# Kernel tuning notes

Measured on AMD Instinct MI355X. Metric: run time of the kernel, lower is better.

Reference implementation:

```python
import jax, jax.numpy as jnp
import numpy as np

VOX = 64      # vox_size
KS = 21       # smooth_ks (odd -> 'SAME' == pad ks//2)
SIGMA = 3.0   # smooth_sigma


def smoothing_kernel():
    # normalized 1D gaussian used separably along the 3 voxel axes
    x = jnp.arange(KS, dtype=jnp.float32) - (KS - 1) / 2.0
    g = jnp.exp(-(x * x) / (2.0 * SIGMA * SIGMA))
    return g / g.sum()


def pc_voxels(pc, size):
    """Trilinear scatter of points in [-0.5,0.5]^3 into a [B,size,size,size] grid."""
    B, N, _ = pc.shape
    g = (pc + 0.5) * (size - 1)            # grid coords
    fl = jnp.floor(g)
    idx = fl.astype(jnp.int32)             # [B,N,3] lower corner
    frac = g - fl                          # trilinear fractions
    # 8 corner offsets in {0,1}^3
    offs = jnp.array([[(i >> 2) & 1, (i >> 1) & 1, i & 1] for i in range(8)], dtype=jnp.int32)
    pos = idx[:, :, None, :] + offs[None, None]                       # [B,N,8,3]
    w = jnp.prod(jnp.where(offs[None, None].astype(bool),
                           frac[:, :, None, :], 1.0 - frac[:, :, None, :]), axis=-1)  # [B,N,8]
    inb = jnp.all((pos >= 0) & (pos < size), axis=-1)
    w = jnp.where(inb, w, 0.0)
    posc = jnp.clip(pos, 0, size - 1)
    # voxel layout vox[b, z, y, x]; pc columns are (x, y, z)
    flat = posc[..., 2] * (size * size) + posc[..., 1] * size + posc[..., 0]
    vox = jnp.zeros((B, size * size * size), pc.dtype)
    vox = vox.at[jnp.arange(B)[:, None, None], flat].add(w)
    return jnp.clip(vox.reshape(B, size, size, size), 0.0, 1.0)


def voxels_smooth(v, g1d, scale):
    """Separable 3D Gaussian smoothing + per-batch scale, clamped to [0,1]."""
    x = v[:, None]  # NCDHW, C=1
    ks = g1d.shape[0]
    for kshape in ((1, 1, ks, 1, 1), (1, 1, 1, ks, 1), (1, 1, 1, 1, ks)):
        x = jax.lax.conv_general_dilated(
            x, g1d.reshape(kshape), (1, 1, 1), 'SAME',
            dimension_numbers=('NCDHW', 'OIDHW', 'NCDHW'))
    x = x[:, 0] * scale[:, None, None, None]
    return jnp.clip(x, 0.0, 1.0)


def drc_prob(v):
    """DRC ray-termination probabilities along depth (axis 1)."""
    trans = jnp.cumprod(1.0 - v, axis=1)                                   # [B,D,H,W]
    tshift = jnp.concatenate([jnp.ones_like(trans[:, :1]), trans[:, :-1]], axis=1)
    stop = v * tshift                                                      # stop at voxel d
    esc = trans[:, -1:]                                                    # ray escapes
    return jnp.concatenate([stop, esc], axis=1)                            # [B,D+1,H,W]


def reference(pc, rotation, scale):
    pc_t = jnp.einsum('bni,bji->bnj', pc, rotation)   # camera transform: pc @ R^T
    vox = pc_voxels(pc_t, VOX)
    sm = voxels_smooth(vox, smoothing_kernel(), scale)
    prob = drc_prob(sm)
    proj = prob[:, :-1].sum(1)[:, ::-1, :]            # sum over depth, flip rows
    return proj


def setup_inputs() -> dict:
    key = jax.random.key(0)
    k1, k2, k3 = jax.random.split(key, 3)
    B, N = 32, 65536
    pc = jax.random.uniform(k1, (B, N, 3), jnp.float32) - 0.5   # points in [-0.5, 0.5]
    q, _ = jnp.linalg.qr(jax.random.normal(k2, (B, 3, 3), jnp.float32))  # random rotations
    scale = 0.5 + jax.random.uniform(k3, (B,), jnp.float32)
    return {"pc": pc, "rotation": q, "scale": scale}
```

## Files before the change

kernel.cpp:

```cpp
#include <hip/hip_runtime.h>

#define NB    32
#define NP    65536
#define SZ    64
#define SZ3   (SZ * SZ * SZ)
#define KS    21
#define HALF  10
#define NBIN2 130
#define CAP2  1280
#define FXS   960.0f

typedef _Float16 half8_t __attribute__((ext_vector_type(8)));
typedef _Float16 half4_t __attribute__((ext_vector_type(4)));
typedef float    f32x4_t __attribute__((ext_vector_type(4)));

__device__ __forceinline__ int swz(int row, int col) {
    return (row << 6) + ((((col >> 3) ^ (row & 7))) << 3) + (col & 7);
}

__device__ __forceinline__ void weights_reg(float* w) {
    float sum = 0.0f;
#pragma unroll
    for (int k = 0; k < KS; ++k) {
        float d = (float)k - (float)HALF;
        w[k] = expf(-d * d / 18.0f);
        sum += w[k];
    }
#pragma unroll
    for (int k = 0; k < KS; ++k) w[k] /= sum;
}

__device__ __forceinline__ void fma4(float4& a, float t, const float4& v) {
    a.x = fmaf(t, v.x, a.x); a.y = fmaf(t, v.y, a.y);
    a.z = fmaf(t, v.z, a.z); a.w = fmaf(t, v.w, a.w);
}

__device__ __forceinline__ unsigned pack_fx(float g) {
    float c = fminf(fmaxf(g, -2.0f), 65.0f);
    return (unsigned)__float2uint_rn((c + 2.0f) * FXS);
}

__global__ void fill_kernel(const float* __restrict__ pc,
                            const float* __restrict__ rot,
                            int* __restrict__ cur,
                            uint2* __restrict__ binned,
                            _Float16* __restrict__ Gg) {
    __shared__ int h[4][NBIN2];
    __shared__ int woff[4][NBIN2];
    __shared__ int lbase[NBIN2];
    int base = blockIdx.x * 1024;
    int b = base >> 16;
    int wv = threadIdx.x >> 6;
    for (int i = threadIdx.x; i < 4 * NBIN2; i += 256) h[i / NBIN2][i % NBIN2] = 0;
    __syncthreads();
    const float* R = rot + b * 9;
    const float4* p4 = (const float4*)(pc + (size_t)base * 3);
    float4 f0 = p4[threadIdx.x * 3 + 0];
    float4 f1 = p4[threadIdx.x * 3 + 1];
    float4 f2 = p4[threadIdx.x * 3 + 2];
    float px[4] = {f0.x, f0.w, f1.z, f2.y};
    float py[4] = {f0.y, f1.x, f1.w, f2.z};
    float pz[4] = {f0.z, f1.y, f2.x, f2.w};
    uint2 pk[4];
    int bin0[4], bin1[4], lp0[4], lp1[4];
#pragma unroll
    for (int j = 0; j < 4; ++j) {
        float g0 = (R[0] * px[j] + R[1] * py[j] + R[2] * pz[j] + 0.5f) * 63.0f;
        float g1 = (R[3] * px[j] + R[4] * py[j] + R[5] * pz[j] + 0.5f) * 63.0f;
        float g2 = (R[6] * px[j] + R[7] * py[j] + R[8] * pz[j] + 0.5f) * 63.0f;
        int i2 = (int)floorf(g2);
        int i1 = (int)floorf(g1);
        bool zv = (i2 >= -1 && i2 <= 63);
        int h0 = ((unsigned)i1       < 64u) ? (i1 >> 5)       : -1;
        int h1 = ((unsigned)(i1 + 1) < 64u) ? ((i1 + 1) >> 5) : -1;
        if (h1 == h0) h1 = -1;
        bin0[j] = (zv && h0 >= 0) ? ((i2 + 1) * 2 + h0) : -1;
        bin1[j] = (zv && h1 >= 0) ? ((i2 + 1) * 2 + h1) : -1;
        pk[j] = make_uint2(pack_fx(g0) | (pack_fx(g1) << 16), pack_fx(g2));
        if (bin0[j] >= 0) lp0[j] = atomicAdd(&h[wv][bin0[j]], 1);
        if (bin1[j] >= 0) lp1[j] = atomicAdd(&h[wv][bin1[j]], 1);
    }
    __syncthreads();
    if (threadIdx.x < NBIN2) {
        int t = threadIdx.x;
        int s0 = h[0][t], s1 = h[1][t], s2 = h[2][t], s3 = h[3][t];
        int tot = s0 + s1 + s2 + s3;
        lbase[t] = tot ? atomicAdd(&cur[b * NBIN2 + t], tot) : 0;
        woff[0][t] = 0; woff[1][t] = s0; woff[2][t] = s0 + s1; woff[3][t] = s0 + s1 + s2;
    }
    __syncthreads();
#pragma unroll
    for (int j = 0; j < 4; ++j) {
        if (bin0[j] >= 0) {
            int pos = lbase[bin0[j]] + woff[wv][bin0[j]] + lp0[j];
            if (pos < CAP2)
                binned[(size_t)(b * NBIN2 + bin0[j]) * CAP2 + pos] = pk[j];
        }
        if (bin1[j] >= 0) {
            int pos = lbase[bin1[j]] + woff[wv][bin1[j]] + lp1[j];
            if (pos < CAP2)
                binned[(size_t)(b * NBIN2 + bin1[j]) * CAP2 + pos] = pk[j];
        }
    }
    if (blockIdx.x == 0) {
        float w[KS];
        weights_reg(w);
        for (int i = threadIdx.x; i < 4096; i += 256) {
            int d = (i >> 6) - (i & 63) + HALF;
            Gg[i] = ((unsigned)d < (unsigned)KS) ? (_Float16)w[d] : (_Float16)0.0f;
        }
    }
}

__global__ void __launch_bounds__(128) splat_blur(const uint2* __restrict__ binned,
                                                  const int* __restrict__ cur,
                                                  const _Float16* __restrict__ Gg,
                                                  _Float16* __restrict__ vox) {
    __shared__ __align__(16) char smem[25088];
    int tid = threadIdx.x;
    int w = tid >> 6, lane = tid & 63;
    int idx = blockIdx.x;
    int b = idx >> 6;
    int k = (idx + (b << 3)) & 63;
    int z = (k & 1) ? (31 - (k >> 1)) : (32 + (k >> 1));
    int q = lane >> 4, c = lane & 15;

    _Float16* Ay = (_Float16*)(smem + w * 4224);
    _Float16* Bx = (_Float16*)(smem + 8448 + w * 8320);
    _Float16* P  = (_Float16*)smem;
    _Float16* T  = (_Float16*)(smem + 8448);

    {
        int4 z4 = {0, 0, 0, 0};
        int4* a4 = (int4*)Ay;
        for (int i = lane; i < 4224 / 16; i += 64) a4[i] = z4;
        int4* b4 = (int4*)Bx;
        for (int i = lane; i < 8320 / 16; i += 64) b4[i] = z4;
    }

    half8_t gf[4][2];
#pragma unroll
    for (int ni = 0; ni < 4; ++ni)
#pragma unroll
        for (int hh = 0; hh < 2; ++hh)
            gf[ni][hh] = *(const half8_t*)&Gg[(ni * 16 + c) * 64 + hh * 32 + q * 8];

    int c0 = min(cur[b * NBIN2 + 2 * z + w],       CAP2);
    int c1 = min(cur[b * NBIN2 + 2 * (z + 1) + w], CAP2);
    const uint2* s0 = binned + (size_t)(b * NBIN2 + 2 * z + w) * CAP2;
    const uint2* s1 = binned + (size_t)(b * NBIN2 + 2 * (z + 1) + w) * CAP2;
    int n = c0 + c1;

    f32x4_t acc[2][4];
#pragma unroll
    for (int ml = 0; ml < 2; ++ml)
#pragma unroll
        for (int ni = 0; ni < 4; ++ni) acc[ml][ni] = (f32x4_t){0.f, 0.f, 0.f, 0.f};

    int iters = (n + 63) >> 6;
    uint2 nxtA = make_uint2(0u, 0u), nxtB = make_uint2(0u, 0u);
    {
        int i0g = lane;
        if (i0g < n) nxtA = (i0g < c0) ? s0[i0g] : s1[i0g - c0];
        int i1g = 64 + lane;
        if (i1g < n) nxtB = (i1g < c0) ? s0[i1g] : s1[i1g - c0];
    }
    for (int it = 0; it < iters; ++it) {
        uint2 pk = nxtA;
        nxtA = nxtB;
        nxtB = make_uint2(0u, 0u);
        int ni2 = (it + 2) * 64 + lane;
        if (ni2 < n) nxtB = (ni2 < c0) ? s0[ni2] : s1[ni2 - c0];

        float gx = (float)(pk.x & 0xffffu) * (1.0f / FXS) - 2.0f;
        float gy = (float)(pk.x >> 16)     * (1.0f / FXS) - 2.0f;
        float gz = (float)(pk.y & 0xffffu) * (1.0f / FXS) - 2.0f;
        float f0 = floorf(gx), f1 = floorf(gy);
        int   i0 = (int)f0,    i1 = (int)f1;
        float r0 = gx - f0,    r1f = gy - f1;
        float az = fmaxf(0.0f, 1.0f - fabsf(gz - (float)z));
        int rlo = i1 - (w << 5), rhi = i1 + 1 - (w << 5);
        int alo = ((unsigned)rlo < 32u) ? rlo : 32;
        int ahi = ((unsigned)rhi < 32u) ? rhi : 32;
        int xlo = ((unsigned)i0       < 64u) ? i0       : 64;
        int xhi = ((unsigned)(i0 + 1) < 64u) ? (i0 + 1) : 64;
        Ay[swz(alo, lane)] = (_Float16)(az * (1.0f - r1f));
        Ay[swz(ahi, lane)] = (_Float16)(az * r1f);
        Bx[swz(xlo, lane)] = (_Float16)(1.0f - r0);
        Bx[swz(xhi, lane)] = (_Float16)r0;
#pragma unroll
        for (int hh = 0; hh < 2; ++hh) {
            half8_t af[2], bf[4];
#pragma unroll
            for (int ml = 0; ml < 2; ++ml)
                af[ml] = *(const half8_t*)&Ay[swz(ml * 16 + c, hh * 32 + q * 8)];
#pragma unroll
            for (int ni = 0; ni < 4; ++ni)
                bf[ni] = *(const half8_t*)&Bx[swz(ni * 16 + c, hh * 32 + q * 8)];
#pragma unroll
            for (int ml = 0; ml < 2; ++ml)
#pragma unroll
                for (int ni = 0; ni < 4; ++ni)
                    acc[ml][ni] = __builtin_amdgcn_mfma_f32_16x16x32_f16(
                        af[ml], bf[ni], acc[ml][ni], 0, 0, 0);
        }
        Ay[swz(alo, lane)] = (_Float16)0.0f;
        Ay[swz(ahi, lane)] = (_Float16)0.0f;
        Bx[swz(xlo, lane)] = (_Float16)0.0f;
        Bx[swz(xhi, lane)] = (_Float16)0.0f;
    }

    __syncthreads();

#pragma unroll
    for (int ml = 0; ml < 2; ++ml)
#pragma unroll
        for (int ni = 0; ni < 4; ++ni)
#pragma unroll
            for (int r = 0; r < 4; ++r)
                P[swz((w << 5) + ml * 16 + q * 4 + r, ni * 16 + c)] =
                    (_Float16)fminf(fmaxf(acc[ml][ni][r], 0.0f), 1.0f);
    __syncthreads();

    f32x4_t a2[2][4];
#pragma unroll
    for (int ml = 0; ml < 2; ++ml)
#pragma unroll
        for (int ni = 0; ni < 4; ++ni) a2[ml][ni] = (f32x4_t){0.f, 0.f, 0.f, 0.f};
#pragma unroll
    for (int hh = 0; hh < 2; ++hh) {
        half8_t af[2];
#pragma unroll
        for (int ml = 0; ml < 2; ++ml)
            af[ml] = *(const half8_t*)&P[swz(((w << 1) + ml) * 16 + c, hh * 32 + q * 8)];
#pragma unroll
        for (int ml = 0; ml < 2; ++ml)
#pragma unroll
            for (int ni = 0; ni < 4; ++ni)
                a2[ml][ni] = __builtin_amdgcn_mfma_f32_16x16x32_f16(
                    af[ml], gf[ni][hh], a2[ml][ni], 0, 0, 0);
    }
#pragma unroll
    for (int ml = 0; ml < 2; ++ml)
#pragma unroll
        for (int ni = 0; ni < 4; ++ni) {
            half4_t pkd;
#pragma unroll
            for (int r = 0; r < 4; ++r) pkd[r] = (_Float16)a2[ml][ni][r];
            *(half4_t*)&T[swz(ni * 16 + c, ((w << 1) + ml) * 16 + q * 4)] = pkd;
        }
    __syncthreads();

    f32x4_t a3[2][4];
#pragma unroll
    for (int ml = 0; ml < 2; ++ml)
#pragma unroll
        for (int ni = 0; ni < 4; ++ni) a3[ml][ni] = (f32x4_t){0.f, 0.f, 0.f, 0.f};
#pragma unroll
    for (int hh = 0; hh < 2; ++hh) {
        half8_t bf[4];
#pragma unroll
        for (int ni = 0; ni < 4; ++ni)
            bf[ni] = *(const half8_t*)&T[swz(ni * 16 + c, hh * 32 + q * 8)];
#pragma unroll
        for (int ml = 0; ml < 2; ++ml)
#pragma unroll
            for (int ni = 0; ni < 4; ++ni)
                a3[ml][ni] = __builtin_amdgcn_mfma_f32_16x16x32_f16(
                    gf[(w << 1) + ml][hh], bf[ni], a3[ml][ni], 0, 0, 0);
    }

    _Float16* dst = vox + ((size_t)b << 18) + ((size_t)z << 12);
#pragma unroll
    for (int ml = 0; ml < 2; ++ml)
#pragma unroll
        for (int ni = 0; ni < 4; ++ni)
#pragma unroll
            for (int r = 0; r < 4; ++r)
                dst[(((w << 5) + ml * 16 + q * 4 + r) << 6) + ni * 16 + c] =
                    (_Float16)a3[ml][ni][r];
}

__global__ void convz_drc_kernel(const _Float16* __restrict__ in,
                                 const float* __restrict__ scale,
                                 float* __restrict__ out) {
    __shared__ float sraw[640 + SZ * SZ + 640];
    __shared__ float c[SZ * SZ];
    __shared__ float segS[4][64], segT[4][64];
    float* s = sraw + 640;
    int b = blockIdx.x >> 6, y = blockIdx.x & 63;

    for (int i = threadIdx.x; i < 640; i += 256) {
        sraw[i] = 0.0f;
        sraw[640 + SZ * SZ + i] = 0.0f;
    }
    const _Float16* base = in + ((size_t)b << 18) + (y << 6);
#pragma unroll
    for (int g = 0; g < 4; ++g) {
        int cell = g * 256 + threadIdx.x;
        int z = cell >> 4, xc = (cell & 15) << 2;
        half4_t v = *(const half4_t*)&base[((size_t)z << 12) + xc];
        float4 f = make_float4((float)v[0], (float)v[1], (float)v[2], (float)v[3]);
        *(float4*)&s[(z << 6) + xc] = f;
    }
    __syncthreads();

    float w[KS];
    weights_reg(w);

    {
        int z0 = (threadIdx.x >> 4) << 2;
        int xc = (threadIdx.x & 15) << 2;
        float4 a0 = {0,0,0,0}, a1 = {0,0,0,0}, a2 = {0,0,0,0}, a3 = {0,0,0,0};
#pragma unroll
        for (int d = 0; d < 24; ++d) {
            int zz = z0 - HALF + d;
            float4 v = *(const float4*)&s[(zz << 6) + xc];
            if (d <= 20)           fma4(a0, w[d],     v);
            if (d >= 1 && d <= 21) fma4(a1, w[d - 1], v);
            if (d >= 2 && d <= 22) fma4(a2, w[d - 2], v);
            if (d >= 3)            fma4(a3, w[d - 3], v);
        }
        *(float4*)&c[((z0 + 0) << 6) + xc] = a0;
        *(float4*)&c[((z0 + 1) << 6) + xc] = a1;
        *(float4*)&c[((z0 + 2) << 6) + xc] = a2;
        *(float4*)&c[((z0 + 3) << 6) + xc] = a3;
    }
    __syncthreads();

    {
        int x = threadIdx.x & 63, seg = threadIdx.x >> 6;
        float sc = scale[b];
        float trans = 1.0f, sum = 0.0f;
#pragma unroll
        for (int zz = 0; zz < 16; ++zz) {
            int z = seg * 16 + zz;
            float v = fminf(fmaxf(c[(z << 6) + x] * sc, 0.0f), 1.0f);
            sum += v * trans;
            trans *= 1.0f - v;
        }
        segS[seg][x] = sum;
        segT[seg][x] = trans;
    }
    __syncthreads();
    if (threadIdx.x < 64) {
        int x = threadIdx.x;
        float t = 1.0f, S = 0.0f;
#pragma unroll
        for (int sgi = 0; sgi < 4; ++sgi) { S += segS[sgi][x] * t; t *= segT[sgi][x]; }
        out[(b << 12) + ((63 - y) << 6) + x] = S;
    }
}

extern "C" void kernel_launch(void* const* d_in, const int* in_sizes, int n_in,
                              void* d_out, int out_size, void* d_ws, size_t ws_size,
                              hipStream_t stream) {
    const float* pc    = (const float*)d_in[0];
    const float* rot   = (const float*)d_in[1];
    const float* scale = (const float*)d_in[2];
    float* out = (float*)d_out;

    _Float16* vox    = (_Float16*)d_ws;
    uint2*    binned = (uint2*)((char*)d_ws + (size_t)NB * SZ3 * sizeof(_Float16));
    _Float16* Gg     = (_Float16*)((char*)binned + (size_t)NB * NBIN2 * CAP2 * sizeof(uint2));
    int*      cur    = (int*)((char*)Gg + 64 * 64 * sizeof(_Float16));

    hipMemsetAsync(cur, 0, NB * NBIN2 * sizeof(int), stream);

    fill_kernel     <<<NB * NP / 1024, 256, 0, stream>>>(pc, rot, cur, binned, Gg);
    splat_blur      <<<NB * SZ, 128, 0, stream>>>(binned, cur, Gg, vox);
    convz_drc_kernel<<<NB * SZ, 256, 0, stream>>>(vox, scale, out);
}
```

Baseline: 123.8 us.

## Bin points into 32x32 quadrants and use four waves per splat block

```diff
diff --git a/kernel.cpp b/kernel.cpp
--- a/kernel.cpp
+++ b/kernel.cpp
@@ -6,8 +6,8 @@
 #define SZ3   (SZ * SZ * SZ)
 #define KS    21
 #define HALF  10
-#define NBIN2 130
-#define CAP2  1280
+#define NBINQ 260
+#define CAPQ  1024
 #define FXS   960.0f
 
 typedef _Float16 half8_t __attribute__((ext_vector_type(8)));
@@ -45,13 +45,13 @@
                             int* __restrict__ cur,
                             uint2* __restrict__ binned,
                             _Float16* __restrict__ Gg) {
-    __shared__ int h[4][NBIN2];
-    __shared__ int woff[4][NBIN2];
-    __shared__ int lbase[NBIN2];
+    __shared__ int hist[4][NBINQ];
+    __shared__ int woff[4][NBINQ];
+    __shared__ int lbase[NBINQ];
     int base = blockIdx.x * 1024;
     int b = base >> 16;
     int wv = threadIdx.x >> 6;
-    for (int i = threadIdx.x; i < 4 * NBIN2; i += 256) h[i / NBIN2][i % NBIN2] = 0;
+    for (int i = threadIdx.x; i < 4 * NBINQ; i += 256) ((int*)hist)[i] = 0;
     __syncthreads();
     const float* R = rot + b * 9;
     const float4* p4 = (const float4*)(pc + (size_t)base * 3);
@@ -62,46 +62,48 @@
     float py[4] = {f0.y, f1.x, f1.w, f2.z};
     float pz[4] = {f0.z, f1.y, f2.x, f2.w};
     uint2 pk[4];
-    int bin0[4], bin1[4], lp0[4], lp1[4];
+    int bn[16], lp[16];
 #pragma unroll
     for (int j = 0; j < 4; ++j) {
         float g0 = (R[0] * px[j] + R[1] * py[j] + R[2] * pz[j] + 0.5f) * 63.0f;
         float g1 = (R[3] * px[j] + R[4] * py[j] + R[5] * pz[j] + 0.5f) * 63.0f;
         float g2 = (R[6] * px[j] + R[7] * py[j] + R[8] * pz[j] + 0.5f) * 63.0f;
-        int i2 = (int)floorf(g2);
-        int i1 = (int)floorf(g1);
+        int i2 = (int)floorf(g2), i1 = (int)floorf(g1), i0 = (int)floorf(g0);
         bool zv = (i2 >= -1 && i2 <= 63);
-        int h0 = ((unsigned)i1       < 64u) ? (i1 >> 5)       : -1;
-        int h1 = ((unsigned)(i1 + 1) < 64u) ? ((i1 + 1) >> 5) : -1;
-        if (h1 == h0) h1 = -1;
-        bin0[j] = (zv && h0 >= 0) ? ((i2 + 1) * 2 + h0) : -1;
-        bin1[j] = (zv && h1 >= 0) ? ((i2 + 1) * 2 + h1) : -1;
+        int ys[2], xs[2];
+        ys[0] = ((unsigned)i1       < 64u) ? (i1 >> 5)       : -1;
+        ys[1] = ((unsigned)(i1 + 1) < 64u) ? ((i1 + 1) >> 5) : -1;
+        if (ys[1] == ys[0]) ys[1] = -1;
+        xs[0] = ((unsigned)i0       < 64u) ? (i0 >> 5)       : -1;
+        xs[1] = ((unsigned)(i0 + 1) < 64u) ? ((i0 + 1) >> 5) : -1;
+        if (xs[1] == xs[0]) xs[1] = -1;
         pk[j] = make_uint2(pack_fx(g0) | (pack_fx(g1) << 16), pack_fx(g2));
-        if (bin0[j] >= 0) lp0[j] = atomicAdd(&h[wv][bin0[j]], 1);
-        if (bin1[j] >= 0) lp1[j] = atomicAdd(&h[wv][bin1[j]], 1);
-    }
-    __syncthreads();
-    if (threadIdx.x < NBIN2) {
-        int t = threadIdx.x;
-        int s0 = h[0][t], s1 = h[1][t], s2 = h[2][t], s3 = h[3][t];
+#pragma unroll
+        for (int cy = 0; cy < 2; ++cy)
+#pragma unroll
+            for (int cx = 0; cx < 2; ++cx) {
+                int kk = j * 4 + cy * 2 + cx;
+                int bb = (zv && ys[cy] >= 0 && xs[cx] >= 0)
+                         ? ((i2 + 1) * 4 + ys[cy] * 2 + xs[cx]) : -1;
+                bn[kk] = bb;
+                lp[kk] = (bb >= 0) ? atomicAdd(&hist[wv][bb], 1) : 0;
+            }
+    }
+    __syncthreads();
+    for (int t = threadIdx.x; t < NBINQ; t += 256) {
+        int s0 = hist[0][t], s1 = hist[1][t], s2 = hist[2][t], s3 = hist[3][t];
         int tot = s0 + s1 + s2 + s3;
-        lbase[t] = tot ? atomicAdd(&cur[b * NBIN2 + t], tot) : 0;
+        lbase[t] = tot ? atomicAdd(&cur[b * NBINQ + t], tot) : 0;
         woff[0][t] = 0; woff[1][t] = s0; woff[2][t] = s0 + s1; woff[3][t] = s0 + s1 + s2;
     }
     __syncthreads();
 #pragma unroll
-    for (int j = 0; j < 4; ++j) {
-        if (bin0[j] >= 0) {
-            int pos = lbase[bin0[j]] + woff[wv][bin0[j]] + lp0[j];
-            if (pos < CAP2)
-                binned[(size_t)(b * NBIN2 + bin0[j]) * CAP2 + pos] = pk[j];
-        }
-        if (bin1[j] >= 0) {
-            int pos = lbase[bin1[j]] + woff[wv][bin1[j]] + lp1[j];
-            if (pos < CAP2)
-                binned[(size_t)(b * NBIN2 + bin1[j]) * CAP2 + pos] = pk[j];
-        }
-    }
+    for (int kk = 0; kk < 16; ++kk)
+        if (bn[kk] >= 0) {
+            int pos = lbase[bn[kk]] + woff[wv][bn[kk]] + lp[kk];
+            if (pos < CAPQ)
+                binned[(size_t)(b * NBINQ + bn[kk]) * CAPQ + pos] = pk[kk >> 2];
+        }
     if (blockIdx.x == 0) {
         float w[KS];
         weights_reg(w);
@@ -112,11 +114,11 @@
     }
 }
 
-__global__ void __launch_bounds__(128) splat_blur(const uint2* __restrict__ binned,
+__global__ void __launch_bounds__(256) splat_blur(const uint2* __restrict__ binned,
                                                   const int* __restrict__ cur,
                                                   const _Float16* __restrict__ Gg,
                                                   _Float16* __restrict__ vox) {
-    __shared__ __align__(16) char smem[25088];
+    __shared__ __align__(16) char smem[4 * 8448];
     int tid = threadIdx.x;
     int w = tid >> 6, lane = tid & 63;
     int idx = blockIdx.x;
@@ -124,18 +126,17 @@
     int k = (idx + (b << 3)) & 63;
     int z = (k & 1) ? (31 - (k >> 1)) : (32 + (k >> 1));
     int q = lane >> 4, c = lane & 15;
-
-    _Float16* Ay = (_Float16*)(smem + w * 4224);
-    _Float16* Bx = (_Float16*)(smem + 8448 + w * 8320);
+    int yh = w >> 1, xh = w & 1;
+
+    _Float16* Ay = (_Float16*)(smem + w * 8448);
+    _Float16* Bx = (_Float16*)(smem + w * 8448 + 4224);
     _Float16* P  = (_Float16*)smem;
     _Float16* T  = (_Float16*)(smem + 8448);
 
     {
         int4 z4 = {0, 0, 0, 0};
-        int4* a4 = (int4*)Ay;
-        for (int i = lane; i < 4224 / 16; i += 64) a4[i] = z4;
-        int4* b4 = (int4*)Bx;
-        for (int i = lane; i < 8320 / 16; i += 64) b4[i] = z4;
+        int4* a4 = (int4*)(smem + w * 8448);
+        for (int i = lane; i < 528; i += 64) a4[i] = z4;
     }
 
     half8_t gf[4][2];
@@ -145,26 +146,24 @@
         for (int hh = 0; hh < 2; ++hh)
             gf[ni][hh] = *(const half8_t*)&Gg[(ni * 16 + c) * 64 + hh * 32 + q * 8];
 
-    int c0 = min(cur[b * NBIN2 + 2 * z + w],       CAP2);
-    int c1 = min(cur[b * NBIN2 + 2 * (z + 1) + w], CAP2);
-    const uint2* s0 = binned + (size_t)(b * NBIN2 + 2 * z + w) * CAP2;
-    const uint2* s1 = binned + (size_t)(b * NBIN2 + 2 * (z + 1) + w) * CAP2;
+    int b0 = b * NBINQ + z * 4 + w;
+    int b1 = b * NBINQ + (z + 1) * 4 + w;
+    int c0 = min(cur[b0], CAPQ);
+    int c1 = min(cur[b1], CAPQ);
+    const uint2* s0 = binned + (size_t)b0 * CAPQ;
+    const uint2* s1 = binned + (size_t)b1 * CAPQ;
     int n = c0 + c1;
 
-    f32x4_t acc[2][4];
+    f32x4_t acc[2][2];
 #pragma unroll
     for (int ml = 0; ml < 2; ++ml)
 #pragma unroll
-        for (int ni = 0; ni < 4; ++ni) acc[ml][ni] = (f32x4_t){0.f, 0.f, 0.f, 0.f};
+        for (int ni = 0; ni < 2; ++ni) acc[ml][ni] = (f32x4_t){0.f, 0.f, 0.f, 0.f};
 
     int iters = (n + 63) >> 6;
     uint2 nxtA = make_uint2(0u, 0u), nxtB = make_uint2(0u, 0u);
-    {
-        int i0g = lane;
-        if (i0g < n) nxtA = (i0g < c0) ? s0[i0g] : s1[i0g - c0];
-        int i1g = 64 + lane;
-        if (i1g < n) nxtB = (i1g < c0) ? s0[i1g] : s1[i1g - c0];
-    }
+    if (lane < n)      nxtA = (lane < c0)      ? s0[lane]      : s1[lane - c0];
+    if (64 + lane < n) nxtB = (64 + lane < c0) ? s0[64 + lane] : s1[64 + lane - c0];
     for (int it = 0; it < iters; ++it) {
         uint2 pk = nxtA;
         nxtA = nxtB;
@@ -179,35 +178,36 @@
         int   i0 = (int)f0,    i1 = (int)f1;
         float r0 = gx - f0,    r1f = gy - f1;
         float az = fmaxf(0.0f, 1.0f - fabsf(gz - (float)z));
-        int rlo = i1 - (w << 5), rhi = i1 + 1 - (w << 5);
+        int rlo = i1 - (yh << 5), rhi = rlo + 1;
         int alo = ((unsigned)rlo < 32u) ? rlo : 32;
         int ahi = ((unsigned)rhi < 32u) ? rhi : 32;
-        int xlo = ((unsigned)i0       < 64u) ? i0       : 64;
-        int xhi = ((unsigned)(i0 + 1) < 64u) ? (i0 + 1) : 64;
+        int clo = i0 - (xh << 5), chi = clo + 1;
+        int blo = ((unsigned)clo < 32u) ? clo : 32;
+        int bhi = ((unsigned)chi < 32u) ? chi : 32;
         Ay[swz(alo, lane)] = (_Float16)(az * (1.0f - r1f));
         Ay[swz(ahi, lane)] = (_Float16)(az * r1f);
-        Bx[swz(xlo, lane)] = (_Float16)(1.0f - r0);
-        Bx[swz(xhi, lane)] = (_Float16)r0;
+        Bx[swz(blo, lane)] = (_Float16)(1.0f - r0);
+        Bx[swz(bhi, lane)] = (_Float16)r0;
 #pragma unroll
         for (int hh = 0; hh < 2; ++hh) {
-            half8_t af[2], bf[4];
+            half8_t af[2], bf[2];
 #pragma unroll
             for (int ml = 0; ml < 2; ++ml)
                 af[ml] = *(const half8_t*)&Ay[swz(ml * 16 + c, hh * 32 + q * 8)];
 #pragma unroll
-            for (int ni = 0; ni < 4; ++ni)
+            for (int ni = 0; ni < 2; ++ni)
                 bf[ni] = *(const half8_t*)&Bx[swz(ni * 16 + c, hh * 32 + q * 8)];
 #pragma unroll
             for (int ml = 0; ml < 2; ++ml)
 #pragma unroll
-                for (int ni = 0; ni < 4; ++ni)
+                for (int ni = 0; ni < 2; ++ni)
                     acc[ml][ni] = __builtin_amdgcn_mfma_f32_16x16x32_f16(
                         af[ml], bf[ni], acc[ml][ni], 0, 0, 0);
         }
         Ay[swz(alo, lane)] = (_Float16)0.0f;
         Ay[swz(ahi, lane)] = (_Float16)0.0f;
-        Bx[swz(xlo, lane)] = (_Float16)0.0f;
-        Bx[swz(xhi, lane)] = (_Float16)0.0f;
+        Bx[swz(blo, lane)] = (_Float16)0.0f;
+        Bx[swz(bhi, lane)] = (_Float16)0.0f;
     }
 
     __syncthreads();
@@ -215,47 +215,35 @@
 #pragma unroll
     for (int ml = 0; ml < 2; ++ml)
 #pragma unroll
+        for (int ni = 0; ni < 2; ++ni)
+#pragma unroll
+            for (int r = 0; r < 4; ++r)
+                P[swz((yh << 5) + ml * 16 + q * 4 + r, (xh << 5) + ni * 16 + c)] =
+                    (_Float16)fminf(fmaxf(acc[ml][ni][r], 0.0f), 1.0f);
+    __syncthreads();
+
+    f32x4_t a2[4];
+#pragma unroll
+    for (int ni = 0; ni < 4; ++ni) a2[ni] = (f32x4_t){0.f, 0.f, 0.f, 0.f};
+#pragma unroll
+    for (int hh = 0; hh < 2; ++hh) {
+        half8_t af = *(const half8_t*)&P[swz(w * 16 + c, hh * 32 + q * 8)];
+#pragma unroll
         for (int ni = 0; ni < 4; ++ni)
-#pragma unroll
-            for (int r = 0; r < 4; ++r)
-                P[swz((w << 5) + ml * 16 + q * 4 + r, ni * 16 + c)] =
-                    (_Float16)fminf(fmaxf(acc[ml][ni][r], 0.0f), 1.0f);
-    __syncthreads();
-
-    f32x4_t a2[2][4];
-#pragma unroll
-    for (int ml = 0; ml < 2; ++ml)
-#pragma unroll
-        for (int ni = 0; ni < 4; ++ni) a2[ml][ni] = (f32x4_t){0.f, 0.f, 0.f, 0.f};
-#pragma unroll
-    for (int hh = 0; hh < 2; ++hh) {
-        half8_t af[2];
-#pragma unroll
-        for (int ml = 0; ml < 2; ++ml)
-            af[ml] = *(const half8_t*)&P[swz(((w << 1) + ml) * 16 + c, hh * 32 + q * 8)];
-#pragma unroll
-        for (int ml = 0; ml < 2; ++ml)
-#pragma unroll
-            for (int ni = 0; ni < 4; ++ni)
-                a2[ml][ni] = __builtin_amdgcn_mfma_f32_16x16x32_f16(
-                    af[ml], gf[ni][hh], a2[ml][ni], 0, 0, 0);
-    }
-#pragma unroll
-    for (int ml = 0; ml < 2; ++ml)
-#pragma unroll
-        for (int ni = 0; ni < 4; ++ni) {
-            half4_t pkd;
-#pragma unroll
-            for (int r = 0; r < 4; ++r) pkd[r] = (_Float16)a2[ml][ni][r];
-            *(half4_t*)&T[swz(ni * 16 + c, ((w << 1) + ml) * 16 + q * 4)] = pkd;
-        }
-    __syncthreads();
-
-    f32x4_t a3[2][4];
-#pragma unroll
-    for (int ml = 0; ml < 2; ++ml)
-#pragma unroll
-        for (int ni = 0; ni < 4; ++ni) a3[ml][ni] = (f32x4_t){0.f, 0.f, 0.f, 0.f};
+            a2[ni] = __builtin_amdgcn_mfma_f32_16x16x32_f16(af, gf[ni][hh], a2[ni], 0, 0, 0);
+    }
+#pragma unroll
+    for (int ni = 0; ni < 4; ++ni) {
+        half4_t pkd;
+#pragma unroll
+        for (int r = 0; r < 4; ++r) pkd[r] = (_Float16)a2[ni][r];
+        *(half4_t*)&T[swz(ni * 16 + c, w * 16 + q * 4)] = pkd;
+    }
+    __syncthreads();
+
+    f32x4_t a3[4];
+#pragma unroll
+    for (int ni = 0; ni < 4; ++ni) a3[ni] = (f32x4_t){0.f, 0.f, 0.f, 0.f};
 #pragma unroll
     for (int hh = 0; hh < 2; ++hh) {
         half8_t bf[4];
@@ -263,22 +251,16 @@
         for (int ni = 0; ni < 4; ++ni)
             bf[ni] = *(const half8_t*)&T[swz(ni * 16 + c, hh * 32 + q * 8)];
 #pragma unroll
-        for (int ml = 0; ml < 2; ++ml)
-#pragma unroll
-            for (int ni = 0; ni < 4; ++ni)
-                a3[ml][ni] = __builtin_amdgcn_mfma_f32_16x16x32_f16(
-                    gf[(w << 1) + ml][hh], bf[ni], a3[ml][ni], 0, 0, 0);
+        for (int ni = 0; ni < 4; ++ni)
+            a3[ni] = __builtin_amdgcn_mfma_f32_16x16x32_f16(gf[w][hh], bf[ni], a3[ni], 0, 0, 0);
     }
 
     _Float16* dst = vox + ((size_t)b << 18) + ((size_t)z << 12);
 #pragma unroll
-    for (int ml = 0; ml < 2; ++ml)
-#pragma unroll
-        for (int ni = 0; ni < 4; ++ni)
-#pragma unroll
-            for (int r = 0; r < 4; ++r)
-                dst[(((w << 5) + ml * 16 + q * 4 + r) << 6) + ni * 16 + c] =
-                    (_Float16)a3[ml][ni][r];
+    for (int ni = 0; ni < 4; ++ni)
+#pragma unroll
+        for (int r = 0; r < 4; ++r)
+            dst[((w * 16 + q * 4 + r) << 6) + ni * 16 + c] = (_Float16)a3[ni][r];
 }
 
 __global__ void convz_drc_kernel(const _Float16* __restrict__ in,
@@ -362,12 +344,12 @@
 
     _Float16* vox    = (_Float16*)d_ws;
     uint2*    binned = (uint2*)((char*)d_ws + (size_t)NB * SZ3 * sizeof(_Float16));
-    _Float16* Gg     = (_Float16*)((char*)binned + (size_t)NB * NBIN2 * CAP2 * sizeof(uint2));
+    _Float16* Gg     = (_Float16*)((char*)binned + (size_t)NB * NBINQ * CAPQ * sizeof(uint2));
     int*      cur    = (int*)((char*)Gg + 64 * 64 * sizeof(_Float16));
 
-    hipMemsetAsync(cur, 0, NB * NBIN2 * sizeof(int), stream);
+    hipMemsetAsync(cur, 0, NB * NBINQ * sizeof(int), stream);
 
     fill_kernel     <<<NB * NP / 1024, 256, 0, stream>>>(pc, rot, cur, binned, Gg);
-    splat_blur      <<<NB * SZ, 128, 0, stream>>>(binned, cur, Gg, vox);
+    splat_blur      <<<NB * SZ, 256, 0, stream>>>(binned, cur, Gg, vox);
     convz_drc_kernel<<<NB * SZ, 256, 0, stream>>>(vox, scale, out);
 }
```

New measurement: 137.7 us. 11.2% more time.
